# Kernel optimization log

Hardware: AMD Instinct MI355X
Metric: run time of the kernel (lower is better)

## Reference

```python
import jax, jax.numpy as jnp
import numpy as np

B, N, K, CIN, COUT, H = 4, 2048, 32, 16, 32, 32
EPS = 1e-5


def setup_inputs() -> dict:
    key = jax.random.key(0)
    ks = jax.random.split(key, 6)
    s = 0.1
    return dict(
        xyz=jax.random.uniform(ks[0], (B, N, 3), dtype=jnp.float32),
        points=jax.random.normal(ks[1], (B, N, CIN), dtype=jnp.float32),
        W1=jax.random.normal(ks[2], (3, H), dtype=jnp.float32) * s,
        b1=jnp.zeros((H,), jnp.float32),
        g1=jnp.ones((H,), jnp.float32),
        be1=jnp.zeros((H,), jnp.float32),
        W2=jax.random.normal(ks[3], (H, H), dtype=jnp.float32) * s,
        b2=jnp.zeros((H,), jnp.float32),
        g2=jnp.ones((H,), jnp.float32),
        be2=jnp.zeros((H,), jnp.float32),
        W3=jax.random.normal(ks[4], (H, CIN * COUT), dtype=jnp.float32) * s,
        b3=jnp.zeros((CIN * COUT,), jnp.float32),
        gbn=jnp.ones((COUT,), jnp.float32),
        bbn=jnp.zeros((COUT,), jnp.float32),
    )


def _bn(h, g, b):
    # BatchNorm1d training-mode math: biased batch stats over axis 0
    return g * (h - h.mean(0)) / jnp.sqrt(h.var(0) + EPS) + b


def reference(xyz, points, W1, b1, g1, be1, W2, b2, g2, be2, W3, b3, gbn, bbn):
    # KNN: squared distances (B,N,N)
    sq = jnp.sum(xyz * xyz, -1)
    dist = -2.0 * jnp.einsum('bmc,bnc->bmn', xyz, xyz) + sq[:, :, None] + sq[:, None, :]
    _, idx = jax.lax.top_k(-dist, K)  # (B,N,K) nearest neighbors

    gather = jax.vmap(lambda p, i: p[i])  # (N,C),(N,K)->(N,K,C), vmapped over B
    grouped_xyz = gather(xyz, idx)                      # (B,N,K,3)
    rel = grouped_xyz - xyz[:, :, None, :]              # (B,N,K,3)
    grouped_pts = gather(points, idx)                   # (B,N,K,CIN)

    # weight net on relative coords
    h = rel.reshape(-1, 3)
    h = _bn(jax.nn.relu(h @ W1 + b1), g1, be1)
    h = _bn(jax.nn.relu(h @ W2 + b2), g2, be2)
    w = (h @ W3 + b3).reshape(B, N, K, CIN, COUT)       # (B,N,K,CIN,COUT)

    # weighted sum over C_in, then max over neighbors
    out = jnp.einsum('bnkc,bnkco->bnko', grouped_pts, w)  # (B,N,K,COUT)
    out = out.max(axis=2)                                 # (B,N,COUT)

    # final BatchNorm1d over (B,N) per channel
    m = out.mean((0, 1))
    v = out.var((0, 1))
    return gbn * (out - m) / jnp.sqrt(v + EPS) + bbn
```

## Files before the change

### kernel.cpp

```cpp
#include <hip/hip_runtime.h>

#define B_ 4
#define N_ 2048
#define K_ 32
#define CIN_ 16
#define COUT_ 32
#define H_ 32
#define R_ (B_*N_*K_)
#define EPS_ 1e-5f
#define INVR_ (1.0f/(float)R_)
#define INVBN_ (1.0f/(float)(B_*N_))
#define LISTCAP 160
#define NSH 16

typedef __attribute__((ext_vector_type(8)))  _Float16 f16x8;
typedef __attribute__((ext_vector_type(2)))  __fp16   hw16x2;
typedef __attribute__((ext_vector_type(2)))  _Float16 f16x2;
typedef __attribute__((ext_vector_type(16))) float    f32x16;

__device__ __forceinline__ float dot3f(float ax,float ay,float az,float bx,float by,float bz){
    return fmaf(az,bz, fmaf(ay,by, ax*bx));
}
__device__ __forceinline__ unsigned int pk2(float a, float b){
    union { hw16x2 v; unsigned int u; } c;
    c.v = __builtin_amdgcn_cvt_pkrtz(a, b);
    return c.u;
}
__device__ __forceinline__ unsigned int pkmul(unsigned int a, unsigned int b){
    union { unsigned int u; f16x2 v; } x, y, r;
    x.u = a; y.u = b; r.v = x.v * y.v; return r.u;
}
__device__ __forceinline__ float shsum(const float* __restrict__ p, int k){
    float s = 0.f;
    #pragma unroll
    for (int i = 0; i < NSH; ++i) s += p[i*32 + k];
    return s;
}

__global__ __launch_bounds__(256) void k_prep0(const float* __restrict__ xyz, float4* __restrict__ xs4g,
                                               float* __restrict__ st){
    int i = blockIdx.x*256 + threadIdx.x;
    float x = xyz[3*i], y = xyz[3*i+1], z = xyz[3*i+2];
    xs4g[i] = make_float4(x, y, z, dot3f(x,y,z,x,y,z));
    if (blockIdx.x == 0){
        for (int j = threadIdx.x; j < 1152; j += 256) st[j] = 0.f;
    }
}

__global__ __launch_bounds__(256,7) void k_knn(const float4* __restrict__ xs4g,
                                               const float* __restrict__ W1, const float* __restrict__ b1,
                                               int* __restrict__ idx_out,
                                               float* __restrict__ s1sh, float* __restrict__ q1sh,
                                               unsigned int* __restrict__ h1f){
    __shared__ unsigned int hist[4][512][2];
    __shared__ unsigned long long lst[4][LISTCAP];
    __shared__ int kidx[4][K_];

    const int tid  = threadIdx.x;
    const int w    = tid >> 6;
    const int lane = tid & 63;
    const int half = lane >> 5;
    const int b    = blockIdx.x >> 9;
    const int q    = ((blockIdx.x & 511) << 2) + w;
    const int bN   = b * N_;
    unsigned int* hw = &hist[w][0][0];

    const uint4 z4 = make_uint4(0,0,0,0);
    uint4* h4 = (uint4*)hw;
    #pragma unroll
    for (int i = 0; i < 4; ++i) h4[i*64 + lane] = z4;

    const float4 qp = xs4g[bN + q];
    const float qx = qp.x, qy = qp.y, qz = qp.z, sqq = qp.w;

    unsigned int fv[32];
    #pragma unroll
    for (int j = 0; j < 32; ++j){
        int c = j*64 + lane;
        float4 pt = xs4g[bN + c];
        float d = fmaf(-2.0f, dot3f(qx,qy,qz, pt.x,pt.y,pt.z), sqq) + pt.w;
        fv[j] = __float_as_uint(d);
        unsigned int u1 = __float_as_uint(d + 1.0f);
        unsigned int key = (u1 <= 0x3F800000u) ? 0u : ((u1 - 0x3F800000u) >> 15);
        key = key > 511u ? 511u : key;
        atomicAdd(&hw[key*2 + (lane & 1)], 1u);
    }

    unsigned int g[8];
    #pragma unroll
    for (int t = 0; t < 4; ++t){
        uint4 h = ((const uint4*)hw)[lane*4 + t];
        g[2*t]   = h.x + h.y;
        g[2*t+1] = h.z + h.w;
    }
    unsigned int gs = 0;
    #pragma unroll
    for (int t = 0; t < 8; ++t) gs += g[t];
    unsigned int cum = gs;
    #pragma unroll
    for (int off = 1; off < 64; off <<= 1){
        unsigned int v = __shfl_up(cum, off);
        if (lane >= off) cum += v;
    }
    unsigned long long bal = __ballot(cum >= (unsigned)K_);
    int L = __ffsll(bal) - 1;
    unsigned int run = __shfl(cum, L) - __shfl(gs, L);
    int Bsel = 8*L + 7;
    {
        unsigned int c = run; bool fnd = false;
        #pragma unroll
        for (int t = 0; t < 8; ++t){
            unsigned int ht = __shfl(g[t], L, 64);
            if (!fnd && c + ht >= (unsigned)K_){ Bsel = 8*L + t; fnd = true; }
            c += ht;
        }
    }
    const float Tedge = __uint_as_float(0x3F800000u + ((unsigned)(Bsel + 1) << 15));
    const bool allin = (Bsel == 511);

    const unsigned long long mlt = (lane == 63) ? ~0ull >> 1 : (1ull << lane) - 1ull;
    unsigned int cnt = 0;
    #pragma unroll
    for (int j = 0; j < 32; ++j){
        float f1 = __uint_as_float(fv[j]) + 1.0f;
        bool surv = (f1 < Tedge) || allin;
        unsigned long long sb = __ballot(surv);
        unsigned int pos = cnt + (unsigned int)__popcll(sb & mlt);
        if (surv && pos < (unsigned)LISTCAP)
            lst[w][pos] = ((unsigned long long)fv[j] << 32) | (unsigned int)(j*64 + lane);
        cnt += (unsigned int)__popcll(sb);
    }
    int m = (int)cnt; if (m > LISTCAP) m = LISTCAP;

    int* outp = idx_out + ((size_t)bN + q) * K_;
    for (int i = lane; i < m; i += 64){
        unsigned long long my = lst[w][i];
        int rank = 0;
        for (int jj = 0; jj < m; ++jj)
            rank += (lst[w][jj] < my) ? 1 : 0;
        if (rank < K_){
            int id = (int)(unsigned int)(my & 0xFFFFFFFFull);
            outp[rank] = id;
            kidx[w][rank] = id;
        }
    }

    {
        const int ch = lane & 31;
        float w1a = W1[ch], w1b = W1[H_+ch], w1c = W1[2*H_+ch], b1c = b1[ch];
        float s = 0.f, qq = 0.f;
        #pragma unroll
        for (int r = 0; r < 16; ++r){
            int idr = kidx[w][half*16 + r];
            float4 pn = xs4g[bN + idr];
            float rx = pn.x - qx, ry = pn.y - qy, rz = pn.z - qz;
            float h = fmaxf(fmaf(rx, w1a, fmaf(ry, w1b, fmaf(rz, w1c, b1c))), 0.0f);
            s += h; qq = fmaf(h, h, qq);
        }
        s  += __shfl_xor(s, 32, 64);
        qq += __shfl_xor(qq, 32, 64);
        if (lane < 32){
            int sh = (blockIdx.x & (NSH-1)) * 32 + ch;
            atomicAdd(&s1sh[sh], s);
            atomicAdd(&q1sh[sh], qq);
        }
    }

    {
        const int id = kidx[w][lane & 31];
        float4 pn = xs4g[bN + id];
        float rx = pn.x - qx, ry = pn.y - qy, rz = pn.z - qz;
        uint4* dst = (uint4*)h1f + (size_t)(bN + q)*128 + lane;
        const int c0 = half*8;
        #pragma unroll
        for (int sblk = 0; sblk < 2; ++sblk){
            const int cb = sblk*16 + c0;
            const float4 wa0 = *(const float4*)(W1 + cb);
            const float4 wa1 = *(const float4*)(W1 + cb + 4);
            const float4 wb0 = *(const float4*)(W1 + H_ + cb);
            const float4 wb1 = *(const float4*)(W1 + H_ + cb + 4);
            const float4 wc0 = *(const float4*)(W1 + 2*H_ + cb);
            const float4 wc1 = *(const float4*)(W1 + 2*H_ + cb + 4);
            const float4 bv0 = *(const float4*)(b1 + cb);
            const float4 bv1 = *(const float4*)(b1 + cb + 4);
            float h0 = fmaxf(fmaf(rx, wa0.x, fmaf(ry, wb0.x, fmaf(rz, wc0.x, bv0.x))), 0.0f);
            float h1v= fmaxf(fmaf(rx, wa0.y, fmaf(ry, wb0.y, fmaf(rz, wc0.y, bv0.y))), 0.0f);
            float h2v= fmaxf(fmaf(rx, wa0.z, fmaf(ry, wb0.z, fmaf(rz, wc0.z, bv0.z))), 0.0f);
            float h3 = fmaxf(fmaf(rx, wa0.w, fmaf(ry, wb0.w, fmaf(rz, wc0.w, bv0.w))), 0.0f);
            float h4 = fmaxf(fmaf(rx, wa1.x, fmaf(ry, wb1.x, fmaf(rz, wc1.x, bv1.x))), 0.0f);
            float h5 = fmaxf(fmaf(rx, wa1.y, fmaf(ry, wb1.y, fmaf(rz, wc1.y, bv1.y))), 0.0f);
            float h6 = fmaxf(fmaf(rx, wa1.z, fmaf(ry, wb1.z, fmaf(rz, wc1.z, bv1.z))), 0.0f);
            float h7 = fmaxf(fmaf(rx, wa1.w, fmaf(ry, wb1.w, fmaf(rz, wc1.w, bv1.w))), 0.0f);
            uint4 o;
            o.x = pk2(h0, h1v); o.y = pk2(h2v, h3); o.z = pk2(h4, h5); o.w = pk2(h6, h7);
            dst[sblk*64] = o;
        }
    }
}

__global__ __launch_bounds__(256) void k_prep2(const float* __restrict__ points,
                                               const float* __restrict__ s1s, const float* __restrict__ q1s,
                                               const float* __restrict__ g1, const float* __restrict__ be1,
                                               const float* __restrict__ W2, const float* __restrict__ b2,
                                               unsigned int* __restrict__ pf16, unsigned int* __restrict__ W2f,
                                               float* __restrict__ b2p){
    int flat = blockIdx.x*256 + threadIdx.x;
    if (flat < 65536){
        pf16[flat] = pk2(points[2*flat], points[2*flat+1]);
    } else if (flat < 66048){
        int d = flat - 65536;
        int jj = d & 3, lane = (d >> 2) & 63, s = d >> 8;
        int col = lane & 31;
        int k0 = s*16 + (lane >> 5)*8 + 2*jj;
        float m0 = shsum(s1s,k0)*INVR_,   v0 = shsum(q1s,k0)*INVR_   - m0*m0;
        float m1 = shsum(s1s,k0+1)*INVR_, v1 = shsum(q1s,k0+1)*INVR_ - m1*m1;
        float a0  = g1[k0]   / sqrtf(v0 + EPS_);
        float a1v = g1[k0+1] / sqrtf(v1 + EPS_);
        W2f[d] = pk2(a0*W2[k0*H_ + col], a1v*W2[(k0+1)*H_ + col]);
    } else if (flat < 66080){
        int col = flat - 66048;
        float acc = b2[col];
        #pragma unroll 4
        for (int h = 0; h < H_; ++h){
            float mm = shsum(s1s,h)*INVR_, vv = shsum(q1s,h)*INVR_ - mm*mm;
            float aa = g1[h] / sqrtf(vv + EPS_);
            float bb = fmaf(-aa, mm, be1[h]);
            acc = fmaf(bb, W2[h*H_ + col], acc);
        }
        b2p[col] = acc;
    }
}

__global__ __launch_bounds__(256,4) void k_h2stats(const uint4* __restrict__ h1f,
                                                   const uint4* __restrict__ W2f, const float* __restrict__ b2p,
                                                   float* gsum, float* gsq){
    __shared__ float redS[H_], redQ[H_];
    const int tid = threadIdx.x, lane = tid & 63, w = tid >> 6;
    const int m = lane & 31;
    if (tid < H_){ redS[tid] = 0.f; redQ[tid] = 0.f; }
    __syncthreads();

    union { uint4 u4; f16x8 v; } Bf0, Bf1;
    Bf0.u4 = W2f[lane];
    Bf1.u4 = W2f[64 + lane];
    float b2c = b2p[m];
    const int blk0 = blockIdx.x*8 + w*2;

    float s = 0.f, q = 0.f;
    #pragma unroll
    for (int t = 0; t < 2; ++t){
        union { uint4 u4; f16x8 v; } a0, a1f;
        a0.u4  = h1f[(size_t)(blk0 + t)*128 + lane];
        a1f.u4 = h1f[(size_t)(blk0 + t)*128 + 64 + lane];
        f32x16 acc;
        #pragma unroll
        for (int i = 0; i < 16; ++i) acc[i] = b2c;
        acc = __builtin_amdgcn_mfma_f32_32x32x16_f16(a0.v,  Bf0.v, acc, 0, 0, 0);
        acc = __builtin_amdgcn_mfma_f32_32x32x16_f16(a1f.v, Bf1.v, acc, 0, 0, 0);
        #pragma unroll
        for (int i = 0; i < 16; ++i){
            float v = fmaxf(acc[i], 0.0f);
            s += v; q = fmaf(v, v, q);
        }
    }
    s += __shfl_xor(s, 32, 64);
    q += __shfl_xor(q, 32, 64);
    if (lane < 32){ atomicAdd(&redS[m], s); atomicAdd(&redQ[m], q); }
    __syncthreads();
    if (tid < H_){ atomicAdd(&gsum[tid], redS[tid]); atomicAdd(&gsq[tid], redQ[tid]); }
}

__global__ __launch_bounds__(256) void k_prep3(const float* __restrict__ W3, const float* __restrict__ b3,
                                               const float* __restrict__ s2, const float* __restrict__ q2,
                                               const float* __restrict__ g2, const float* __restrict__ be2,
                                               unsigned int* __restrict__ W3f){
    int d = blockIdx.x*256 + threadIdx.x;
    int jj = d & 3, lane = (d >> 2) & 63, step = d >> 8;
    int col = lane & 31;
    int off = (lane >> 5)*8 + 2*jj;
    float v0, v1;
    if (step < 32){
        int h = step, c0 = off;
        float mm = s2[h]*INVR_, vv = q2[h]*INVR_ - mm*mm;
        float aa = g2[h] / sqrtf(vv + EPS_);
        v0 = aa * W3[h*512 + c0*COUT_ + col];
        v1 = aa * W3[h*512 + (c0+1)*COUT_ + col];
    } else {
        int c0 = off;
        v0 = b3[c0*COUT_ + col]; v1 = b3[(c0+1)*COUT_ + col];
        #pragma unroll 4
        for (int h = 0; h < H_; ++h){
            float mm = s2[h]*INVR_, vv = q2[h]*INVR_ - mm*mm;
            float aa = g2[h] / sqrtf(vv + EPS_);
            float bb = fmaf(-aa, mm, be2[h]);
            v0 = fmaf(bb, W3[h*512 + c0*COUT_ + col], v0);
            v1 = fmaf(bb, W3[h*512 + (c0+1)*COUT_ + col], v1);
        }
    }
    W3f[d] = pk2(v0, v1);
}

__global__ __launch_bounds__(256,4) void k_out(const uint4* __restrict__ h1f, const int* __restrict__ idx,
                                               const uint4* __restrict__ W2f, const float* __restrict__ b2p,
                                               const unsigned int* __restrict__ pf16,
                                               const uint4* __restrict__ W3f,
                                               float* __restrict__ out_pre, float* gsum, float* gsq){
    __shared__ uint4 Wls[2112];
    __shared__ float redS[COUT_], redQ[COUT_];
    const int tid = threadIdx.x, lane = tid & 63, w = tid >> 6;
    const int half = lane >> 5, m = lane & 31;
    for (int i = tid; i < 2112; i += 256) Wls[i] = W3f[i];
    if (tid < COUT_){ redS[tid] = 0.f; redQ[tid] = 0.f; }
    __syncthreads();

    const int rB = blockIdx.x*256 + w*64;
    const int blk0 = blockIdx.x*8 + w*2;

    union { uint4 u4; f16x8 v; } A0, A1;
    A0.u4 = W2f[lane];
    A1.u4 = W2f[64 + lane];

    #pragma unroll
    for (int t = 0; t < 2; ++t){
        union { uint4 u4; f16x8 v; } B0f, B1f;
        B0f.u4 = h1f[(size_t)(blk0 + t)*128 + lane];
        B1f.u4 = h1f[(size_t)(blk0 + t)*128 + 64 + lane];

        f32x16 c2;
        #pragma unroll
        for (int i = 0; i < 16; ++i) c2[i] = b2p[(i&3) + 8*(i>>2) + 4*half];
        c2 = __builtin_amdgcn_mfma_f32_32x32x16_f16(A0.v, B0f.v, c2, 0, 0, 0);
        c2 = __builtin_amdgcn_mfma_f32_32x32x16_f16(A1.v, B1f.v, c2, 0, 0, 0);

        unsigned int h2p[16];
        #pragma unroll
        for (int p = 0; p < 8; ++p){
            float v0 = fmaxf(c2[2*p],   0.0f);
            float v1 = fmaxf(c2[2*p+1], 0.0f);
            unsigned int ow = pk2(v0, v1);
            unsigned int ot = __shfl_xor(ow, 32, 64);
            int a = p >> 1, bb = p & 1;
            h2p[4*a + 2*half     + bb] = ow;
            h2p[4*a + 2*(1-half) + bb] = ot;
        }

        int row = rB + t*32 + m;
        int bb_ = row >> 16;
        int idr = idx[row];
        const uint4* gpp = (const uint4*)(pf16 + ((size_t)bb_*N_ + idr)*8);
        uint4 ga = gpp[0], gb = gpp[1];
        unsigned int gsel[4];
        gsel[0] = half ? gb.x : ga.x;
        gsel[1] = half ? gb.y : ga.y;
        gsel[2] = half ? gb.z : ga.z;
        gsel[3] = half ? gb.w : ga.w;

        f32x16 acc;
        #pragma unroll
        for (int i = 0; i < 16; ++i) acc[i] = 0.f;
        #pragma unroll
        for (int kb = 0; kb < 32; ++kb){
            unsigned int hr = h2p[kb >> 1];
            unsigned int hd = __builtin_amdgcn_perm(hr, hr, (kb & 1) ? 0x03020302u : 0x01000100u);
            union { unsigned int u[4]; f16x8 v; } af;
            #pragma unroll
            for (int jj = 0; jj < 4; ++jj) af.u[jj] = pkmul(hd, gsel[jj]);
            union { uint4 u4; f16x8 v; } bf; bf.u4 = Wls[kb*64 + lane];
            acc = __builtin_amdgcn_mfma_f32_32x32x16_f16(af.v, bf.v, acc, 0, 0, 0);
        }
        {
            union { unsigned int u[4]; f16x8 v; } af;
            #pragma unroll
            for (int jj = 0; jj < 4; ++jj) af.u[jj] = gsel[jj];
            union { uint4 u4; f16x8 v; } bf; bf.u4 = Wls[32*64 + lane];
            acc = __builtin_amdgcn_mfma_f32_32x32x16_f16(af.v, bf.v, acc, 0, 0, 0);
        }

        float v = acc[0];
        #pragma unroll
        for (int i = 1; i < 16; ++i) v = fmaxf(v, acc[i]);
        v = fmaxf(v, __shfl_xor(v, 32, 64));
        if (lane < 32){
            int g = blockIdx.x*8 + w*2 + t;
            out_pre[(size_t)g*COUT_ + m] = v;
            atomicAdd(&redS[m], v);
            atomicAdd(&redQ[m], v*v);
        }
    }
    __syncthreads();
    if (tid < COUT_){ atomicAdd(&gsum[tid], redS[tid]); atomicAdd(&gsq[tid], redQ[tid]); }
}

__global__ __launch_bounds__(256) void k_bn(const float* __restrict__ out_pre,
                                            const float* __restrict__ s3, const float* __restrict__ q3,
                                            const float* __restrict__ gbn, const float* __restrict__ bbn,
                                            float* __restrict__ out){
    int i = blockIdx.x*256 + threadIdx.x;
    int o = i & (COUT_-1);
    float mm = s3[o] * INVBN_;
    float vv = q3[o] * INVBN_ - mm*mm;
    float aa = gbn[o] / sqrtf(vv + EPS_);
    out[i] = fmaf(aa, out_pre[i], fmaf(-aa, mm, bbn[o]));
}

extern "C" void kernel_launch(void* const* d_in, const int* in_sizes, int n_in,
                              void* d_out, int out_size, void* d_ws, size_t ws_size,
                              hipStream_t stream){
    const float* xyz    = (const float*)d_in[0];
    const float* points = (const float*)d_in[1];
    const float* W1  = (const float*)d_in[2];
    const float* b1  = (const float*)d_in[3];
    const float* g1  = (const float*)d_in[4];
    const float* be1 = (const float*)d_in[5];
    const float* W2  = (const float*)d_in[6];
    const float* b2  = (const float*)d_in[7];
    const float* g2  = (const float*)d_in[8];
    const float* be2 = (const float*)d_in[9];
    const float* W3  = (const float*)d_in[10];
    const float* b3  = (const float*)d_in[11];
    const float* gbn = (const float*)d_in[12];
    const float* bbn = (const float*)d_in[13];
    float* out = (float*)d_out;

    char* base = (char*)d_ws;
    int*            idx     = (int*)(base + 0);
    float*          out_pre = (float*)(base + 1048576);
    unsigned int*   pf16    = (unsigned int*)(base + 2097152);
    unsigned int*   W3f     = (unsigned int*)(base + 2359296);
    unsigned int*   W2f     = (unsigned int*)(base + 2393088);
    float*          b2p     = (float*)(base + 2395136);
    float*          st      = (float*)(base + 2395264);
    float4*         xs4g    = (float4*)(base + 2399872);
    unsigned int*   h1f     = (unsigned int*)(base + 4194304);
    float *s1s=st, *q1s=st+512, *s2=st+1024, *q2=st+1056, *s3=st+1088, *q3=st+1120;

    hipLaunchKernelGGL(k_prep0,   dim3(32),      dim3(256), 0, stream, xyz, xs4g, st);
    hipLaunchKernelGGL(k_knn,     dim3(B_*N_/4), dim3(256), 0, stream, xs4g, W1, b1, idx, s1s, q1s, h1f);
    hipLaunchKernelGGL(k_prep2,   dim3(260),     dim3(256), 0, stream, points, s1s, q1s, g1, be1, W2, b2,
                       pf16, W2f, b2p);
    hipLaunchKernelGGL(k_h2stats, dim3(R_/256),  dim3(256), 0, stream, (const uint4*)h1f,
                       (const uint4*)W2f, b2p, s2, q2);
    hipLaunchKernelGGL(k_prep3,   dim3(33),      dim3(256), 0, stream, W3, b3, s2, q2, g2, be2, W3f);
    hipLaunchKernelGGL(k_out,     dim3(R_/256),  dim3(256), 0, stream, (const uint4*)h1f, idx,
                       (const uint4*)W2f, b2p, pf16, (const uint4*)W3f, out_pre, s3, q3);
    hipLaunchKernelGGL(k_bn,      dim3(B_*N_*COUT_/256), dim3(256), 0, stream, out_pre, s3, q3, gbn, bbn, out);
}
```

Before: 181.0 us.

## Fold prep kernels into last-block tails and interleave k_out MFMA chains

Removes the k_prep2 and k_prep3 launches. The points fp16 conversion moves into k_prep0, and the W2/W3 folding with the BN statistics now runs in the last block of k_knn and of k_h2stats, found with an atomic counter and threadfence. k_out is also restructured so the two tiles' gathers and first-layer MFMAs are issued up front, and their second-layer MFMA chains are interleaved for more instruction-level parallelism. This trades two kernel launches and their gaps for a serial tail in one block, plus extra register pressure in k_out.

Result: slower. 417.2 us (+130.5%).

```diff
diff --git a/kernel.cpp b/kernel.cpp
--- a/kernel.cpp
+++ b/kernel.cpp
@@ -12,6 +12,8 @@
 #define INVBN_ (1.0f/(float)(B_*N_))
 #define LISTCAP 160
 #define NSH 16
+#define GRID_KNN (B_*N_/4)
+#define GRID_H2  (R_/256)
 
 typedef __attribute__((ext_vector_type(8)))  _Float16 f16x8;
 typedef __attribute__((ext_vector_type(2)))  __fp16   hw16x2;
@@ -30,31 +32,37 @@
     union { unsigned int u; f16x2 v; } x, y, r;
     x.u = a; y.u = b; r.v = x.v * y.v; return r.u;
 }
-__device__ __forceinline__ float shsum(const float* __restrict__ p, int k){
-    float s = 0.f;
-    #pragma unroll
-    for (int i = 0; i < NSH; ++i) s += p[i*32 + k];
-    return s;
-}
-
-__global__ __launch_bounds__(256) void k_prep0(const float* __restrict__ xyz, float4* __restrict__ xs4g,
+
+__global__ __launch_bounds__(256) void k_prep0(const float* __restrict__ xyz, const float* __restrict__ points,
+                                               float4* __restrict__ xs4g, unsigned int* __restrict__ pf16,
                                                float* __restrict__ st){
-    int i = blockIdx.x*256 + threadIdx.x;
-    float x = xyz[3*i], y = xyz[3*i+1], z = xyz[3*i+2];
-    xs4g[i] = make_float4(x, y, z, dot3f(x,y,z,x,y,z));
+    int flat = blockIdx.x*256 + threadIdx.x;
+    if (flat < 8192){
+        float x = xyz[3*flat], y = xyz[3*flat+1], z = xyz[3*flat+2];
+        xs4g[flat] = make_float4(x, y, z, dot3f(x,y,z,x,y,z));
+    } else {
+        int p = flat - 8192;
+        pf16[p] = pk2(points[2*p], points[2*p+1]);
+    }
     if (blockIdx.x == 0){
-        for (int j = threadIdx.x; j < 1152; j += 256) st[j] = 0.f;
+        for (int j = threadIdx.x; j < 1280; j += 256) st[j] = 0.f;
     }
 }
 
 __global__ __launch_bounds__(256,7) void k_knn(const float4* __restrict__ xs4g,
                                                const float* __restrict__ W1, const float* __restrict__ b1,
+                                               const float* __restrict__ g1, const float* __restrict__ be1,
+                                               const float* __restrict__ W2, const float* __restrict__ b2,
                                                int* __restrict__ idx_out,
                                                float* __restrict__ s1sh, float* __restrict__ q1sh,
-                                               unsigned int* __restrict__ h1f){
+                                               unsigned int* __restrict__ h1f,
+                                               unsigned int* __restrict__ W2f, float* __restrict__ b2p,
+                                               int* __restrict__ cnt){
     __shared__ unsigned int hist[4][512][2];
     __shared__ unsigned long long lst[4][LISTCAP];
     __shared__ int kidx[4][K_];
+    __shared__ float tailA[H_], tailB[H_];
+    __shared__ int lastS;
 
     const int tid  = threadIdx.x;
     const int w    = tid >> 6;
@@ -119,18 +127,18 @@
     const bool allin = (Bsel == 511);
 
     const unsigned long long mlt = (lane == 63) ? ~0ull >> 1 : (1ull << lane) - 1ull;
-    unsigned int cnt = 0;
+    unsigned int cnt2 = 0;
     #pragma unroll
     for (int j = 0; j < 32; ++j){
         float f1 = __uint_as_float(fv[j]) + 1.0f;
         bool surv = (f1 < Tedge) || allin;
         unsigned long long sb = __ballot(surv);
-        unsigned int pos = cnt + (unsigned int)__popcll(sb & mlt);
+        unsigned int pos = cnt2 + (unsigned int)__popcll(sb & mlt);
         if (surv && pos < (unsigned)LISTCAP)
             lst[w][pos] = ((unsigned long long)fv[j] << 32) | (unsigned int)(j*64 + lane);
-        cnt += (unsigned int)__popcll(sb);
-    }
-    int m = (int)cnt; if (m > LISTCAP) m = LISTCAP;
+        cnt2 += (unsigned int)__popcll(sb);
+    }
+    int m = (int)cnt2; if (m > LISTCAP) m = LISTCAP;
 
     int* outp = idx_out + ((size_t)bN + q) * K_;
     for (int i = lane; i < m; i += 64){
@@ -196,45 +204,52 @@
             dst[sblk*64] = o;
         }
     }
-}
-
-__global__ __launch_bounds__(256) void k_prep2(const float* __restrict__ points,
-                                               const float* __restrict__ s1s, const float* __restrict__ q1s,
-                                               const float* __restrict__ g1, const float* __restrict__ be1,
-                                               const float* __restrict__ W2, const float* __restrict__ b2,
-                                               unsigned int* __restrict__ pf16, unsigned int* __restrict__ W2f,
-                                               float* __restrict__ b2p){
-    int flat = blockIdx.x*256 + threadIdx.x;
-    if (flat < 65536){
-        pf16[flat] = pk2(points[2*flat], points[2*flat+1]);
-    } else if (flat < 66048){
-        int d = flat - 65536;
-        int jj = d & 3, lane = (d >> 2) & 63, s = d >> 8;
-        int col = lane & 31;
-        int k0 = s*16 + (lane >> 5)*8 + 2*jj;
-        float m0 = shsum(s1s,k0)*INVR_,   v0 = shsum(q1s,k0)*INVR_   - m0*m0;
-        float m1 = shsum(s1s,k0+1)*INVR_, v1 = shsum(q1s,k0+1)*INVR_ - m1*m1;
-        float a0  = g1[k0]   / sqrtf(v0 + EPS_);
-        float a1v = g1[k0+1] / sqrtf(v1 + EPS_);
-        W2f[d] = pk2(a0*W2[k0*H_ + col], a1v*W2[(k0+1)*H_ + col]);
-    } else if (flat < 66080){
-        int col = flat - 66048;
-        float acc = b2[col];
-        #pragma unroll 4
-        for (int h = 0; h < H_; ++h){
-            float mm = shsum(s1s,h)*INVR_, vv = shsum(q1s,h)*INVR_ - mm*mm;
-            float aa = g1[h] / sqrtf(vv + EPS_);
-            float bb = fmaf(-aa, mm, be1[h]);
-            acc = fmaf(bb, W2[h*H_ + col], acc);
-        }
-        b2p[col] = acc;
+
+    __threadfence();
+    __syncthreads();
+    if (tid == 0) lastS = (atomicAdd(cnt, 1) == GRID_KNN - 1) ? 1 : 0;
+    __syncthreads();
+    if (lastS){
+        __threadfence();
+        if (tid < H_){
+            float s = 0.f, qq = 0.f;
+            #pragma unroll
+            for (int i = 0; i < NSH; ++i){
+                s  += atomicAdd(&s1sh[i*32 + tid], 0.0f);
+                qq += atomicAdd(&q1sh[i*32 + tid], 0.0f);
+            }
+            float mm = s*INVR_, vv = qq*INVR_ - mm*mm;
+            float aa = g1[tid] / sqrtf(vv + EPS_);
+            tailA[tid] = aa;
+            tailB[tid] = fmaf(-aa, mm, be1[tid]);
+        }
+        __syncthreads();
+        #pragma unroll
+        for (int e = 0; e < 2; ++e){
+            int d = tid*2 + e;
+            int jj = d & 3, ln = (d >> 2) & 63, s = d >> 8;
+            int col = ln & 31;
+            int k0 = s*16 + ((ln >> 5) << 3) + 2*jj;
+            W2f[d] = pk2(tailA[k0]*W2[k0*H_ + col], tailA[k0+1]*W2[(k0+1)*H_ + col]);
+        }
+        if (tid < H_){
+            float acc = b2[tid];
+            #pragma unroll 4
+            for (int h = 0; h < H_; ++h) acc = fmaf(tailB[h], W2[h*H_ + tid], acc);
+            b2p[tid] = acc;
+        }
     }
 }
 
 __global__ __launch_bounds__(256,4) void k_h2stats(const uint4* __restrict__ h1f,
                                                    const uint4* __restrict__ W2f, const float* __restrict__ b2p,
-                                                   float* gsum, float* gsq){
+                                                   float* gsum, float* gsq,
+                                                   const float* __restrict__ W3, const float* __restrict__ b3,
+                                                   const float* __restrict__ g2, const float* __restrict__ be2,
+                                                   unsigned int* __restrict__ W3f, int* __restrict__ cnt){
     __shared__ float redS[H_], redQ[H_];
+    __shared__ float aa2[H_], bb2[H_];
+    __shared__ int lastS;
     const int tid = threadIdx.x, lane = tid & 63, w = tid >> 6;
     const int m = lane & 31;
     if (tid < H_){ redS[tid] = 0.f; redQ[tid] = 0.f; }
@@ -268,37 +283,87 @@
     if (lane < 32){ atomicAdd(&redS[m], s); atomicAdd(&redQ[m], q); }
     __syncthreads();
     if (tid < H_){ atomicAdd(&gsum[tid], redS[tid]); atomicAdd(&gsq[tid], redQ[tid]); }
-}
-
-__global__ __launch_bounds__(256) void k_prep3(const float* __restrict__ W3, const float* __restrict__ b3,
-                                               const float* __restrict__ s2, const float* __restrict__ q2,
-                                               const float* __restrict__ g2, const float* __restrict__ be2,
-                                               unsigned int* __restrict__ W3f){
-    int d = blockIdx.x*256 + threadIdx.x;
-    int jj = d & 3, lane = (d >> 2) & 63, step = d >> 8;
-    int col = lane & 31;
-    int off = (lane >> 5)*8 + 2*jj;
-    float v0, v1;
-    if (step < 32){
-        int h = step, c0 = off;
-        float mm = s2[h]*INVR_, vv = q2[h]*INVR_ - mm*mm;
-        float aa = g2[h] / sqrtf(vv + EPS_);
-        v0 = aa * W3[h*512 + c0*COUT_ + col];
-        v1 = aa * W3[h*512 + (c0+1)*COUT_ + col];
-    } else {
-        int c0 = off;
-        v0 = b3[c0*COUT_ + col]; v1 = b3[(c0+1)*COUT_ + col];
-        #pragma unroll 4
-        for (int h = 0; h < H_; ++h){
-            float mm = s2[h]*INVR_, vv = q2[h]*INVR_ - mm*mm;
-            float aa = g2[h] / sqrtf(vv + EPS_);
-            float bb = fmaf(-aa, mm, be2[h]);
-            v0 = fmaf(bb, W3[h*512 + c0*COUT_ + col], v0);
-            v1 = fmaf(bb, W3[h*512 + (c0+1)*COUT_ + col], v1);
-        }
-    }
-    W3f[d] = pk2(v0, v1);
-}
+
+    __threadfence();
+    __syncthreads();
+    if (tid == 0) lastS = (atomicAdd(cnt, 1) == GRID_H2 - 1) ? 1 : 0;
+    __syncthreads();
+    if (lastS){
+        __threadfence();
+        if (tid < H_){
+            float ss = atomicAdd(&gsum[tid], 0.0f);
+            float qq = atomicAdd(&gsq[tid], 0.0f);
+            float mm = ss*INVR_, vv = qq*INVR_ - mm*mm;
+            float aa = g2[tid] / sqrtf(vv + EPS_);
+            aa2[tid] = aa;
+            bb2[tid] = fmaf(-aa, mm, be2[tid]);
+        }
+        __syncthreads();
+        #pragma unroll 1
+        for (int step = 0; step < 32; ++step){
+            int d = step*256 + tid;
+            int jj = d & 3, ln = (d >> 2) & 63;
+            int col = ln & 31, c0 = ((ln >> 5) << 3) + 2*jj;
+            float a = aa2[step];
+            W3f[d] = pk2(a*W3[step*512 + c0*COUT_ + col], a*W3[step*512 + (c0+1)*COUT_ + col]);
+        }
+        {
+            int d = 32*256 + tid;
+            int jj = d & 3, ln = (d >> 2) & 63;
+            int col = ln & 31, c0 = ((ln >> 5) << 3) + 2*jj;
+            float v0 = b3[c0*COUT_ + col], v1 = b3[(c0+1)*COUT_ + col];
+            #pragma unroll 4
+            for (int h = 0; h < H_; ++h){
+                v0 = fmaf(bb2[h], W3[h*512 + c0*COUT_ + col], v0);
+                v1 = fmaf(bb2[h], W3[h*512 + (c0+1)*COUT_ + col], v1);
+            }
+            W3f[d] = pk2(v0, v1);
+        }
+    }
+}
+
+#define PHASEA(T, H2P, GSEL) do { \
+    union { uint4 u4; f16x8 v; } B0f, B1f; \
+    B0f.u4 = h1f[(size_t)(blk0 + (T))*128 + lane]; \
+    B1f.u4 = h1f[(size_t)(blk0 + (T))*128 + 64 + lane]; \
+    int row = rB + (T)*32 + m; \
+    int bb_ = row >> 16; \
+    int idr = idx[row]; \
+    const uint4* gpp = (const uint4*)(pf16 + ((size_t)bb_*N_ + idr)*8); \
+    uint4 ga = gpp[0], gb = gpp[1]; \
+    GSEL[0] = half ? gb.x : ga.x; \
+    GSEL[1] = half ? gb.y : ga.y; \
+    GSEL[2] = half ? gb.z : ga.z; \
+    GSEL[3] = half ? gb.w : ga.w; \
+    f32x16 c2; \
+    _Pragma("unroll") \
+    for (int i = 0; i < 16; ++i) c2[i] = b2v[i]; \
+    c2 = __builtin_amdgcn_mfma_f32_32x32x16_f16(A0.v, B0f.v, c2, 0, 0, 0); \
+    c2 = __builtin_amdgcn_mfma_f32_32x32x16_f16(A1.v, B1f.v, c2, 0, 0, 0); \
+    _Pragma("unroll") \
+    for (int p = 0; p < 8; ++p){ \
+        float v0 = fmaxf(c2[2*p],   0.0f); \
+        float v1 = fmaxf(c2[2*p+1], 0.0f); \
+        unsigned int ow = pk2(v0, v1); \
+        unsigned int ot = __shfl_xor(ow, 32, 64); \
+        int a = p >> 1, bb = p & 1; \
+        H2P[4*a + bb]     = half ? ot : ow; \
+        H2P[4*a + 2 + bb] = half ? ow : ot; \
+    } \
+} while(0)
+
+#define REDST(ACC, T) do { \
+    float v = ACC[0]; \
+    _Pragma("unroll") \
+    for (int i = 1; i < 16; ++i) v = fmaxf(v, ACC[i]); \
+    v = fmaxf(v, __shfl_xor(v, 32, 64)); \
+    if (lane < 32){ \
+        int g = blk0 + (T); \
+        out_pre[(size_t)g*COUT_ + m] = v; \
+        atomicAdd(&redS[m], v); \
+        atomicAdd(&redQ[m], v*v); \
+    } \
+} while(0)
 
 __global__ __launch_bounds__(256,4) void k_out(const uint4* __restrict__ h1f, const int* __restrict__ idx,
                                                const uint4* __restrict__ W2f, const float* __restrict__ b2p,
@@ -319,74 +384,48 @@
     union { uint4 u4; f16x8 v; } A0, A1;
     A0.u4 = W2f[lane];
     A1.u4 = W2f[64 + lane];
-
-    #pragma unroll
-    for (int t = 0; t < 2; ++t){
-        union { uint4 u4; f16x8 v; } B0f, B1f;
-        B0f.u4 = h1f[(size_t)(blk0 + t)*128 + lane];
-        B1f.u4 = h1f[(size_t)(blk0 + t)*128 + 64 + lane];
-
-        f32x16 c2;
-        #pragma unroll
-        for (int i = 0; i < 16; ++i) c2[i] = b2p[(i&3) + 8*(i>>2) + 4*half];
-        c2 = __builtin_amdgcn_mfma_f32_32x32x16_f16(A0.v, B0f.v, c2, 0, 0, 0);
-        c2 = __builtin_amdgcn_mfma_f32_32x32x16_f16(A1.v, B1f.v, c2, 0, 0, 0);
-
-        unsigned int h2p[16];
-        #pragma unroll
-        for (int p = 0; p < 8; ++p){
-            float v0 = fmaxf(c2[2*p],   0.0f);
-            float v1 = fmaxf(c2[2*p+1], 0.0f);
-            unsigned int ow = pk2(v0, v1);
-            unsigned int ot = __shfl_xor(ow, 32, 64);
-            int a = p >> 1, bb = p & 1;
-            h2p[4*a + 2*half     + bb] = ow;
-            h2p[4*a + 2*(1-half) + bb] = ot;
-        }
-
-        int row = rB + t*32 + m;
-        int bb_ = row >> 16;
-        int idr = idx[row];
-        const uint4* gpp = (const uint4*)(pf16 + ((size_t)bb_*N_ + idr)*8);
-        uint4 ga = gpp[0], gb = gpp[1];
-        unsigned int gsel[4];
-        gsel[0] = half ? gb.x : ga.x;
-        gsel[1] = half ? gb.y : ga.y;
-        gsel[2] = half ? gb.z : ga.z;
-        gsel[3] = half ? gb.w : ga.w;
-
-        f32x16 acc;
-        #pragma unroll
-        for (int i = 0; i < 16; ++i) acc[i] = 0.f;
-        #pragma unroll
-        for (int kb = 0; kb < 32; ++kb){
-            unsigned int hr = h2p[kb >> 1];
-            unsigned int hd = __builtin_amdgcn_perm(hr, hr, (kb & 1) ? 0x03020302u : 0x01000100u);
-            union { unsigned int u[4]; f16x8 v; } af;
-            #pragma unroll
-            for (int jj = 0; jj < 4; ++jj) af.u[jj] = pkmul(hd, gsel[jj]);
-            union { uint4 u4; f16x8 v; } bf; bf.u4 = Wls[kb*64 + lane];
-            acc = __builtin_amdgcn_mfma_f32_32x32x16_f16(af.v, bf.v, acc, 0, 0, 0);
-        }
-        {
-            union { unsigned int u[4]; f16x8 v; } af;
-            #pragma unroll
-            for (int jj = 0; jj < 4; ++jj) af.u[jj] = gsel[jj];
-            union { uint4 u4; f16x8 v; } bf; bf.u4 = Wls[32*64 + lane];
-            acc = __builtin_amdgcn_mfma_f32_32x32x16_f16(af.v, bf.v, acc, 0, 0, 0);
-        }
-
-        float v = acc[0];
-        #pragma unroll
-        for (int i = 1; i < 16; ++i) v = fmaxf(v, acc[i]);
-        v = fmaxf(v, __shfl_xor(v, 32, 64));
-        if (lane < 32){
-            int g = blockIdx.x*8 + w*2 + t;
-            out_pre[(size_t)g*COUT_ + m] = v;
-            atomicAdd(&redS[m], v);
-            atomicAdd(&redQ[m], v*v);
-        }
-    }
+    float b2v[16];
+    #pragma unroll
+    for (int i = 0; i < 16; ++i) b2v[i] = b2p[(i&3) + 8*(i>>2) + 4*half];
+
+    unsigned int h2p0[16], h2p1[16];
+    unsigned int gsel0[4], gsel1[4];
+    PHASEA(0, h2p0, gsel0);
+    PHASEA(1, h2p1, gsel1);
+
+    f32x16 acc0, acc1;
+    #pragma unroll
+    for (int i = 0; i < 16; ++i){ acc0[i] = 0.f; acc1[i] = 0.f; }
+    #pragma unroll
+    for (int kb = 0; kb < 32; ++kb){
+        union { uint4 u4; f16x8 v; } bf; bf.u4 = Wls[kb*64 + lane];
+        const unsigned int sel = (kb & 1) ? 0x03020302u : 0x01000100u;
+        unsigned int hr0 = h2p0[kb >> 1];
+        unsigned int hd0 = __builtin_amdgcn_perm(hr0, hr0, sel);
+        union { unsigned int u[4]; f16x8 v; } af;
+        #pragma unroll
+        for (int jj = 0; jj < 4; ++jj) af.u[jj] = pkmul(hd0, gsel0[jj]);
+        acc0 = __builtin_amdgcn_mfma_f32_32x32x16_f16(af.v, bf.v, acc0, 0, 0, 0);
+        unsigned int hr1 = h2p1[kb >> 1];
+        unsigned int hd1 = __builtin_amdgcn_perm(hr1, hr1, sel);
+        #pragma unroll
+        for (int jj = 0; jj < 4; ++jj) af.u[jj] = pkmul(hd1, gsel1[jj]);
+        acc1 = __builtin_amdgcn_mfma_f32_32x32x16_f16(af.v, bf.v, acc1, 0, 0, 0);
+    }
+    {
+        union { uint4 u4; f16x8 v; } bf; bf.u4 = Wls[32*64 + lane];
+        union { unsigned int u[4]; f16x8 v; } af;
+        #pragma unroll
+        for (int jj = 0; jj < 4; ++jj) af.u[jj] = gsel0[jj];
+        acc0 = __builtin_amdgcn_mfma_f32_32x32x16_f16(af.v, bf.v, acc0, 0, 0, 0);
+        #pragma unroll
+        for (int jj = 0; jj < 4; ++jj) af.u[jj] = gsel1[jj];
+        acc1 = __builtin_amdgcn_mfma_f32_32x32x16_f16(af.v, bf.v, acc1, 0, 0, 0);
+    }
+
+    REDST(acc0, 0);
+    REDST(acc1, 1);
+
     __syncthreads();
     if (tid < COUT_){ atomicAdd(&gsum[tid], redS[tid]); atomicAdd(&gsq[tid], redQ[tid]); }
 }
@@ -430,18 +469,18 @@
     unsigned int*   W2f     = (unsigned int*)(base + 2393088);
     float*          b2p     = (float*)(base + 2395136);
     float*          st      = (float*)(base + 2395264);
-    float4*         xs4g    = (float4*)(base + 2399872);
+    float4*         xs4g    = (float4*)(base + 2400384);
     unsigned int*   h1f     = (unsigned int*)(base + 4194304);
     float *s1s=st, *q1s=st+512, *s2=st+1024, *q2=st+1056, *s3=st+1088, *q3=st+1120;
-
-    hipLaunchKernelGGL(k_prep0,   dim3(32),      dim3(256), 0, stream, xyz, xs4g, st);
-    hipLaunchKernelGGL(k_knn,     dim3(B_*N_/4), dim3(256), 0, stream, xs4g, W1, b1, idx, s1s, q1s, h1f);
-    hipLaunchKernelGGL(k_prep2,   dim3(260),     dim3(256), 0, stream, points, s1s, q1s, g1, be1, W2, b2,
-                       pf16, W2f, b2p);
-    hipLaunchKernelGGL(k_h2stats, dim3(R_/256),  dim3(256), 0, stream, (const uint4*)h1f,
-                       (const uint4*)W2f, b2p, s2, q2);
-    hipLaunchKernelGGL(k_prep3,   dim3(33),      dim3(256), 0, stream, W3, b3, s2, q2, g2, be2, W3f);
-    hipLaunchKernelGGL(k_out,     dim3(R_/256),  dim3(256), 0, stream, (const uint4*)h1f, idx,
+    int *cnt1 = (int*)(st + 1184);
+    int *cnt2 = (int*)(st + 1185);
+
+    hipLaunchKernelGGL(k_prep0,   dim3(288),      dim3(256), 0, stream, xyz, points, xs4g, pf16, st);
+    hipLaunchKernelGGL(k_knn,     dim3(GRID_KNN), dim3(256), 0, stream, xs4g, W1, b1, g1, be1, W2, b2,
+                       idx, s1s, q1s, h1f, W2f, b2p, cnt1);
+    hipLaunchKernelGGL(k_h2stats, dim3(GRID_H2),  dim3(256), 0, stream, (const uint4*)h1f,
+                       (const uint4*)W2f, b2p, s2, q2, W3, b3, g2, be2, W3f, cnt2);
+    hipLaunchKernelGGL(k_out,     dim3(R_/256),   dim3(256), 0, stream, (const uint4*)h1f, idx,
                        (const uint4*)W2f, b2p, pf16, (const uint4*)W3f, out_pre, s3, q3);
     hipLaunchKernelGGL(k_bn,      dim3(B_*N_*COUT_/256), dim3(256), 0, stream, out_pre, s3, q3, gbn, bbn, out);
 }
```
